# Optimization experiments

Measured on AMD Instinct MI355X. Metric: run time of the kernel, lower is better.

## Reference

```python
import jax, jax.numpy as jnp
import numpy as np

B, S, H, M = 32, 512, 1024, 8  # batch, seq_len, HP_hidden_dim, term_span (max span length)


def setup_inputs() -> dict:
    key = jax.random.key(0)
    ks = jax.random.split(key, 6)
    return {
        "hidden_states": jax.random.normal(ks[0], (B, S, H), jnp.float32),
        "term_weight": jax.random.normal(ks[1], (H,), jnp.float32),          # nn.Parameter termWeight
        "w_in": jax.random.normal(ks[2], (H, H), jnp.float32) / np.float32(np.sqrt(H)),  # TermAttention.linear_in weight
        "b_in": jnp.zeros((H,), jnp.float32),                                 # TermAttention.linear_in bias
        "score_w": jax.random.normal(ks[3], (H,), jnp.float32) / np.float32(np.sqrt(H)),  # spanEmb2Score weight
        "score_b": jnp.zeros((), jnp.float32),                                # spanEmb2Score bias
        "seq_lengths": jnp.full((B,), S, jnp.int32),                          # full-length sentences (K is then static)
        "gold_mask": jax.random.randint(ks[4], (B, S, M), 0, 20, jnp.int32),
    }


def reference(hidden_states, term_weight, w_in, b_in, score_w, score_b, seq_lengths, gold_mask):
    B_, S_, H_ = hidden_states.shape
    M_ = gold_mask.shape[-1]

    # TermAttention: query = linear_in(termWeight)
    query = jnp.dot(w_in, term_weight) + b_in  # [H]

    pos = jnp.arange(S_)[:, None] + jnp.arange(M_)[None, :]          # [S, M]
    win = jnp.take(hidden_states, jnp.clip(pos, 0, S_ - 1), axis=1)  # [B, S, M, H]

    # Attention logits: dot(hidden, query), softmax over span positions per span length l+1
    logits = jnp.einsum('bsmh,h->bsm', win, query)                   # [B, S, M]
    m_idx = jnp.arange(M_)
    pos_mask = m_idx[None, :] < (m_idx[:, None] + 1)                 # [L, M]: position m valid for span length l+1
    masked = jnp.where(pos_mask[None, None], logits[:, :, None, :], -jnp.inf)  # [B, S, L, M]
    att = jax.nn.softmax(masked, axis=-1)
    pooled = jnp.einsum('bslm,bsmh->bslh', att, win)                 # [B, S, L, H] attention-pooled span reps

    # spanEmb2Score: Linear(H, 1)
    scores = jnp.einsum('bslh,h->bsl', pooled, score_w) + score_b    # [B, S, L]

    # Valid (deduplicated) spans: (s, s+l+1) kept iff s + l + 1 <= seq_len (matches set-dedup of clipped ends)
    span_valid = (jnp.arange(S_)[None, :, None] + m_idx[None, None, :] + 1) <= seq_lengths[:, None, None]
    gold = (gold_mask == 0) & span_valid

    # SoftMarginLoss: target 1 for gold spans, target 0 for all other spans -> constant log(2) term (faithful)
    per_span = jnp.where(gold, jax.nn.softplus(-scores), jnp.log(2.0).astype(scores.dtype))
    n_valid = jnp.sum(span_valid).astype(scores.dtype)
    loss = jnp.sum(jnp.where(span_valid, per_span, 0.0)) / n_valid

    # Precision@K, K = floor(0.3 * total_words); static since all sentences are full length
    K = int(0.3 * B_ * S_)
    flat_scores = jnp.where(span_valid, scores, -jnp.inf).reshape(-1)
    _, top_idx = jax.lax.top_k(flat_scores, K)
    right = jnp.sum(gold.reshape(-1)[top_idx])
    precision = right / K
    return loss, precision
```

## Files before the change

### kernel.cpp

```cpp
#include <hip/hip_runtime.h>

#define BB 32
#define SS 512
#define HH 1024
#define MM 8
#define NROWS (BB*SS)
#define NSPANS (BB*SS*MM)
#define KSEL 4915

constexpr size_t OFF_QUERY = 0;
constexpr size_t OFF_QD    = 4096;
constexpr size_t OFF_SD    = OFF_QD + 65536;
constexpr size_t OFF_KEYS  = OFF_SD + 65536;
constexpr size_t OFF_GOLD  = OFF_KEYS + 524288;
constexpr size_t OFF_H0    = OFF_GOLD + 524288;
constexpr size_t OFF_H1    = OFF_H0 + 16384;
constexpr size_t OFF_H2    = OFF_H1 + 16384;
constexpr size_t OFF_SCAL  = OFF_H2 + 1024;
constexpr size_t OFF_EQ    = OFF_SCAL + 64;
constexpr unsigned ZERO_WORDS = (unsigned)((OFF_EQ - OFF_H0) / 4);

struct Scal {
    float    loss_sum;
    unsigned n_valid;
    unsigned right_gt;
    unsigned eq_count;
    unsigned done;
};

__device__ __forceinline__ unsigned sortable_key(float f) {
    unsigned b = __float_as_uint(f);
    return (b & 0x80000000u) ? ~b : (b | 0x80000000u);
}

__device__ __forceinline__ void sel4096(const unsigned* __restrict__ gh, unsigned R,
                                        unsigned* sp, unsigned* sres, int tid,
                                        unsigned& c, unsigned& rem) {
    unsigned loc[16]; unsigned lsumv = 0;
    #pragma unroll
    for (int i = 0; i < 16; ++i) { loc[i] = gh[tid * 16 + i]; lsumv += loc[i]; }
    __syncthreads();
    sp[tid] = lsumv;
    __syncthreads();
    #pragma unroll
    for (int off = 1; off < 256; off <<= 1) {
        unsigned v = (tid + off < 256) ? sp[tid + off] : 0u;
        __syncthreads();
        sp[tid] += v;
        __syncthreads();
    }
    unsigned Pt  = sp[tid];
    unsigned Pt1 = (tid < 255) ? sp[tid + 1] : 0u;
    if (Pt >= R && Pt1 < R) {
        unsigned cum = Pt1;
        #pragma unroll
        for (int i = 15; i >= 0; --i) {
            unsigned h = loc[i];
            if (cum + h >= R) { sres[0] = (unsigned)(tid * 16 + i); sres[1] = R - cum; break; }
            cum += h;
        }
    }
    __syncthreads();
    c = sres[0]; rem = sres[1];
    __syncthreads();
}

__device__ __forceinline__ void sel256(const unsigned* __restrict__ gh, unsigned R,
                                       unsigned* sp, unsigned* sres, int tid,
                                       unsigned& c, unsigned& rem) {
    __syncthreads();
    sp[tid] = gh[tid];
    __syncthreads();
    #pragma unroll
    for (int off = 1; off < 256; off <<= 1) {
        unsigned v = (tid + off < 256) ? sp[tid + off] : 0u;
        __syncthreads();
        sp[tid] += v;
        __syncthreads();
    }
    unsigned Pt  = sp[tid];
    unsigned Pt1 = (tid < 255) ? sp[tid + 1] : 0u;
    if (Pt >= R && Pt1 < R) { sres[0] = (unsigned)tid; sres[1] = R - Pt1; }
    __syncthreads();
    c = sres[0]; rem = sres[1];
    __syncthreads();
}

__global__ void k_query(const float* __restrict__ w_in, const float* __restrict__ tw,
                        const float* __restrict__ b_in, char* __restrict__ ws) {
    if (blockIdx.x == 0) {
        unsigned* z = (unsigned*)(ws + OFF_H0);
        for (unsigned i = threadIdx.x; i < ZERO_WORDS; i += 256) z[i] = 0u;
    }
    float* query = (float*)(ws + OFF_QUERY);
    int wave = (blockIdx.x * blockDim.x + threadIdx.x) >> 6;
    int lane = threadIdx.x & 63;
    if (wave >= HH) return;
    const float4* wrow = (const float4*)(w_in + (size_t)wave * HH);
    const float4* tv   = (const float4*)tw;
    float s = 0.f;
    #pragma unroll
    for (int p = 0; p < 4; ++p) {
        int c = p * 64 + lane;
        float4 w = wrow[c]; float4 t = tv[c];
        s += w.x*t.x + w.y*t.y + w.z*t.z + w.w*t.w;
    }
    #pragma unroll
    for (int o = 32; o > 0; o >>= 1) s += __shfl_down(s, o);
    if (lane == 0) query[wave] = s + b_in[wave];
}

__global__ void k_dots(const float* __restrict__ hs, const float* __restrict__ sw,
                       char* __restrict__ ws) {
    const float* query = (const float*)(ws + OFF_QUERY);
    float* qd = (float*)(ws + OFF_QD);
    float* sd = (float*)(ws + OFF_SD);
    int wave = (blockIdx.x * blockDim.x + threadIdx.x) >> 6;
    int lane = threadIdx.x & 63;
    if (wave >= NROWS) return;
    const float4* row = (const float4*)(hs + (size_t)wave * HH);
    const float4* qv  = (const float4*)query;
    const float4* sv  = (const float4*)sw;
    float a = 0.f, c2 = 0.f;
    #pragma unroll
    for (int p = 0; p < 4; ++p) {
        int c = p * 64 + lane;
        float4 h = row[c]; float4 q = qv[c]; float4 w = sv[c];
        a  += h.x*q.x + h.y*q.y + h.z*q.z + h.w*q.w;
        c2 += h.x*w.x + h.y*w.y + h.z*w.z + h.w*w.w;
    }
    #pragma unroll
    for (int o = 32; o > 0; o >>= 1) { a += __shfl_down(a, o); c2 += __shfl_down(c2, o); }
    if (lane == 0) { qd[wave] = a; sd[wave] = c2; }
}

__global__ void k_scores(const int* __restrict__ gold_mask, const int* __restrict__ seq_lengths,
                         const float* __restrict__ score_b_p, char* __restrict__ ws) {
    const float* qd = (const float*)(ws + OFF_QD);
    const float* sd = (const float*)(ws + OFF_SD);
    unsigned* keys  = (unsigned*)(ws + OFF_KEYS);
    unsigned* goldf = (unsigned*)(ws + OFF_GOLD);
    unsigned* h0    = (unsigned*)(ws + OFF_H0);
    Scal*     sc    = (Scal*)(ws + OFF_SCAL);

    __shared__ unsigned hloc[4096];
    __shared__ float lsum[256];
    __shared__ int   lcnt[256];
    for (int i = threadIdx.x; i < 4096; i += 256) hloc[i] = 0;
    __syncthreads();

    int t = blockIdx.x * 256 + threadIdx.x;
    int b = t >> 9, s = t & (SS - 1);
    int seqlen = seq_lengths[b];
    float sb = *score_b_p;

    uint4 gm0 = ((const uint4*)gold_mask)[t * 2];
    uint4 gm1 = ((const uint4*)gold_mask)[t * 2 + 1];
    unsigned gmv[8] = {gm0.x, gm0.y, gm0.z, gm0.w, gm1.x, gm1.y, gm1.z, gm1.w};

    unsigned kbuf[8], gbuf[8];
    float lloss = 0.f; int lval = 0;
    float maxv = 0.f, den = 0.f, num = 0.f;
    #pragma unroll
    for (int m = 0; m < MM; ++m) {
        int pos = s + m; if (pos > SS - 1) pos = SS - 1;
        float x = qd[b * SS + pos];
        float v = sd[b * SS + pos];
        if (m == 0)         { maxv = x; den = 1.f; num = v; }
        else if (x > maxv)  { float e = expf(maxv - x); den = den * e + 1.f; num = num * e + v; maxv = x; }
        else                { float e = expf(x - maxv); den += e; num += e * v; }
        float score = num / den + sb;
        bool valid = (s + m + 1) <= seqlen;
        bool gold  = valid && (gmv[m] == 0u);
        unsigned key = valid ? sortable_key(score) : 0u;
        kbuf[m] = key;
        gbuf[m] = gold ? 1u : 0u;
        if (valid) {
            atomicAdd(&hloc[key >> 20], 1u);
            lval++;
            float z = -score;
            float sp = (z > 0.f) ? (z + log1pf(expf(-z))) : log1pf(expf(z));
            lloss += gold ? sp : 0.69314718055994531f;
        }
    }
    ((uint4*)keys)[t * 2]      = make_uint4(kbuf[0], kbuf[1], kbuf[2], kbuf[3]);
    ((uint4*)keys)[t * 2 + 1]  = make_uint4(kbuf[4], kbuf[5], kbuf[6], kbuf[7]);
    ((uint4*)goldf)[t * 2]     = make_uint4(gbuf[0], gbuf[1], gbuf[2], gbuf[3]);
    ((uint4*)goldf)[t * 2 + 1] = make_uint4(gbuf[4], gbuf[5], gbuf[6], gbuf[7]);

    lsum[threadIdx.x] = lloss; lcnt[threadIdx.x] = lval;
    __syncthreads();
    for (int i = threadIdx.x; i < 4096; i += 256) {
        unsigned v = hloc[i]; if (v) atomicAdd(&h0[i], v);
    }
    for (int o = 128; o > 0; o >>= 1) {
        if (threadIdx.x < o) { lsum[threadIdx.x] += lsum[threadIdx.x + o]; lcnt[threadIdx.x] += lcnt[threadIdx.x + o]; }
        __syncthreads();
    }
    if (threadIdx.x == 0) {
        atomicAdd(&sc->loss_sum, lsum[0]);
        atomicAdd(&sc->n_valid, (unsigned)lcnt[0]);
    }
}

__global__ void k_lvl1(char* __restrict__ ws) {
    const unsigned* keys = (const unsigned*)(ws + OFF_KEYS);
    const unsigned* h0   = (const unsigned*)(ws + OFF_H0);
    unsigned* h1         = (unsigned*)(ws + OFF_H1);
    __shared__ unsigned hloc[4096];
    __shared__ unsigned sp[256];
    __shared__ unsigned sres[2];
    int tid = threadIdx.x;
    unsigned c0, r0;
    sel4096(h0, KSEL, sp, sres, tid, c0, r0);
    for (int i = tid; i < 4096; i += 256) hloc[i] = 0;
    __syncthreads();
    for (int i = blockIdx.x * 256 + tid; i < NSPANS; i += gridDim.x * 256) {
        unsigned k = keys[i];
        if (k != 0u && (k >> 20) == c0) atomicAdd(&hloc[(k >> 8) & 0xFFFu], 1u);
    }
    __syncthreads();
    for (int i = tid; i < 4096; i += 256) {
        unsigned v = hloc[i]; if (v) atomicAdd(&h1[i], v);
    }
}

__global__ void k_lvl2(char* __restrict__ ws) {
    const unsigned* keys = (const unsigned*)(ws + OFF_KEYS);
    const unsigned* h0   = (const unsigned*)(ws + OFF_H0);
    const unsigned* h1   = (const unsigned*)(ws + OFF_H1);
    unsigned* h2         = (unsigned*)(ws + OFF_H2);
    __shared__ unsigned hloc[256];
    __shared__ unsigned sp[256];
    __shared__ unsigned sres[2];
    int tid = threadIdx.x;
    unsigned c0, r0, c1, r1;
    sel4096(h0, KSEL, sp, sres, tid, c0, r0);
    sel4096(h1, r0,   sp, sres, tid, c1, r1);
    unsigned pref = (c0 << 12) | c1;
    hloc[tid] = 0;
    __syncthreads();
    for (int i = blockIdx.x * 256 + tid; i < NSPANS; i += gridDim.x * 256) {
        unsigned k = keys[i];
        if (k != 0u && (k >> 8) == pref) atomicAdd(&hloc[k & 0xFFu], 1u);
    }
    __syncthreads();
    { unsigned v = hloc[tid]; if (v) atomicAdd(&h2[tid], v); }
}

__global__ void k_count_final(char* __restrict__ ws, float* __restrict__ out) {
    const unsigned* keys  = (const unsigned*)(ws + OFF_KEYS);
    const unsigned* goldf = (const unsigned*)(ws + OFF_GOLD);
    const unsigned* h0    = (const unsigned*)(ws + OFF_H0);
    const unsigned* h1    = (const unsigned*)(ws + OFF_H1);
    const unsigned* h2    = (const unsigned*)(ws + OFF_H2);
    unsigned* eqL         = (unsigned*)(ws + OFF_EQ);
    Scal*     sc          = (Scal*)(ws + OFF_SCAL);
    __shared__ unsigned sp[256];
    __shared__ unsigned sres[2];
    __shared__ unsigned is_last;
    int tid = threadIdx.x;
    unsigned c0, r0, c1, r1, c2, r2;
    sel4096(h0, KSEL, sp, sres, tid, c0, r0);
    sel4096(h1, r0,   sp, sres, tid, c1, r1);
    sel256 (h2, r1,   sp, sres, tid, c2, r2);
    unsigned tau = (c0 << 20) | (c1 << 8) | c2;
    unsigned T   = r2;

    int lgt = 0;
    for (int i = blockIdx.x * 256 + tid; i < NSPANS; i += gridDim.x * 256) {
        unsigned k = keys[i];
        if (k > tau) lgt += (int)goldf[i];
        else if (k == tau) {
            unsigned p = atomicAdd(&sc->eq_count, 1u);
            if (p < 4096) atomicExch(&eqL[p], (unsigned)i);
        }
    }
    #pragma unroll
    for (int o = 32; o > 0; o >>= 1) lgt += __shfl_down(lgt, o);
    if ((tid & 63) == 0 && lgt) atomicAdd(&sc->right_gt, (unsigned)lgt);

    __threadfence();
    __syncthreads();
    if (tid == 0) {
        unsigned prev = atomicAdd(&sc->done, 1u);
        is_last = (prev == gridDim.x - 1) ? 1u : 0u;
    }
    __syncthreads();
    if (is_last && tid == 0) {
        __threadfence();
        unsigned neq = __hip_atomic_load(&sc->eq_count, __ATOMIC_RELAXED, __HIP_MEMORY_SCOPE_AGENT);
        if (neq > 4096) neq = 4096;
        unsigned extra = 0;
        if (T >= neq) {
            for (unsigned i = 0; i < neq; ++i) {
                unsigned v = __hip_atomic_load(&eqL[i], __ATOMIC_RELAXED, __HIP_MEMORY_SCOPE_AGENT);
                extra += goldf[v];
            }
        } else {
            unsigned prev2 = 0; bool first = true;
            for (unsigned it = 0; it < T; ++it) {
                unsigned mn = 0xFFFFFFFFu;
                for (unsigned i = 0; i < neq; ++i) {
                    unsigned v = __hip_atomic_load(&eqL[i], __ATOMIC_RELAXED, __HIP_MEMORY_SCOPE_AGENT);
                    if ((first || v > prev2) && v < mn) mn = v;
                }
                if (mn == 0xFFFFFFFFu) break;
                extra += goldf[mn];
                prev2 = mn; first = false;
            }
        }
        float ls = __hip_atomic_load(&sc->loss_sum, __ATOMIC_RELAXED, __HIP_MEMORY_SCOPE_AGENT);
        unsigned nv = __hip_atomic_load(&sc->n_valid, __ATOMIC_RELAXED, __HIP_MEMORY_SCOPE_AGENT);
        unsigned rg = __hip_atomic_load(&sc->right_gt, __ATOMIC_RELAXED, __HIP_MEMORY_SCOPE_AGENT);
        out[0] = ls / (float)nv;
        out[1] = (float)(rg + extra) / (float)KSEL;
    }
}

extern "C" void kernel_launch(void* const* d_in, const int* in_sizes, int n_in,
                              void* d_out, int out_size, void* d_ws, size_t ws_size,
                              hipStream_t stream) {
    const float* hidden   = (const float*)d_in[0];
    const float* term_w   = (const float*)d_in[1];
    const float* w_in     = (const float*)d_in[2];
    const float* b_in     = (const float*)d_in[3];
    const float* score_w  = (const float*)d_in[4];
    const float* score_b  = (const float*)d_in[5];
    const int*   seq_len  = (const int*)d_in[6];
    const int*   gmask    = (const int*)d_in[7];
    float* out            = (float*)d_out;
    char*  ws             = (char*)d_ws;

    k_query      <<<256, 256, 0, stream>>>(w_in, term_w, b_in, ws);
    k_dots       <<<4096, 256, 0, stream>>>(hidden, score_w, ws);
    k_scores     <<<64, 256, 0, stream>>>(gmask, seq_len, score_b, ws);
    k_lvl1       <<<64, 256, 0, stream>>>(ws);
    k_lvl2       <<<64, 256, 0, stream>>>(ws);
    k_count_final<<<64, 256, 0, stream>>>(ws, out);
}
```

Baseline: 142.7 us.

## Replace three-pass radix select with single compaction pass and one-block final select

```diff
diff --git a/kernel.cpp b/kernel.cpp
--- a/kernel.cpp
+++ b/kernel.cpp
@@ -12,20 +12,17 @@
 constexpr size_t OFF_QD    = 4096;
 constexpr size_t OFF_SD    = OFF_QD + 65536;
 constexpr size_t OFF_KEYS  = OFF_SD + 65536;
-constexpr size_t OFF_GOLD  = OFF_KEYS + 524288;
-constexpr size_t OFF_H0    = OFF_GOLD + 524288;
-constexpr size_t OFF_H1    = OFF_H0 + 16384;
-constexpr size_t OFF_H2    = OFF_H1 + 16384;
-constexpr size_t OFF_SCAL  = OFF_H2 + 1024;
-constexpr size_t OFF_EQ    = OFF_SCAL + 64;
-constexpr unsigned ZERO_WORDS = (unsigned)((OFF_EQ - OFF_H0) / 4);
+constexpr size_t OFF_H0    = OFF_KEYS + 524288;
+constexpr size_t OFF_GH    = OFF_H0 + 16384;
+constexpr size_t OFF_SCAL  = OFF_GH + 16384;
+constexpr size_t OFF_CKEY  = OFF_SCAL + 64;
+constexpr size_t OFF_CIDX  = OFF_CKEY + 524288;
+constexpr unsigned ZERO_WORDS = (unsigned)((OFF_SCAL + 64 - OFF_H0) / 4);
 
 struct Scal {
     float    loss_sum;
     unsigned n_valid;
-    unsigned right_gt;
-    unsigned eq_count;
-    unsigned done;
+    unsigned nB;
 };
 
 __device__ __forceinline__ unsigned sortable_key(float f) {
@@ -139,14 +136,15 @@
     const float* qd = (const float*)(ws + OFF_QD);
     const float* sd = (const float*)(ws + OFF_SD);
     unsigned* keys  = (unsigned*)(ws + OFF_KEYS);
-    unsigned* goldf = (unsigned*)(ws + OFF_GOLD);
     unsigned* h0    = (unsigned*)(ws + OFF_H0);
+    unsigned* gh0   = (unsigned*)(ws + OFF_GH);
     Scal*     sc    = (Scal*)(ws + OFF_SCAL);
 
     __shared__ unsigned hloc[4096];
+    __shared__ unsigned gloc[4096];
     __shared__ float lsum[256];
     __shared__ int   lcnt[256];
-    for (int i = threadIdx.x; i < 4096; i += 256) hloc[i] = 0;
+    for (int i = threadIdx.x; i < 4096; i += 256) { hloc[i] = 0; gloc[i] = 0; }
     __syncthreads();
 
     int t = blockIdx.x * 256 + threadIdx.x;
@@ -158,7 +156,7 @@
     uint4 gm1 = ((const uint4*)gold_mask)[t * 2 + 1];
     unsigned gmv[8] = {gm0.x, gm0.y, gm0.z, gm0.w, gm1.x, gm1.y, gm1.z, gm1.w};
 
-    unsigned kbuf[8], gbuf[8];
+    unsigned kbuf[8];
     float lloss = 0.f; int lval = 0;
     float maxv = 0.f, den = 0.f, num = 0.f;
     #pragma unroll
@@ -174,9 +172,9 @@
         bool gold  = valid && (gmv[m] == 0u);
         unsigned key = valid ? sortable_key(score) : 0u;
         kbuf[m] = key;
-        gbuf[m] = gold ? 1u : 0u;
         if (valid) {
             atomicAdd(&hloc[key >> 20], 1u);
+            if (gold) atomicAdd(&gloc[key >> 20], 1u);
             lval++;
             float z = -score;
             float sp = (z > 0.f) ? (z + log1pf(expf(-z))) : log1pf(expf(z));
@@ -185,13 +183,12 @@
     }
     ((uint4*)keys)[t * 2]      = make_uint4(kbuf[0], kbuf[1], kbuf[2], kbuf[3]);
     ((uint4*)keys)[t * 2 + 1]  = make_uint4(kbuf[4], kbuf[5], kbuf[6], kbuf[7]);
-    ((uint4*)goldf)[t * 2]     = make_uint4(gbuf[0], gbuf[1], gbuf[2], gbuf[3]);
-    ((uint4*)goldf)[t * 2 + 1] = make_uint4(gbuf[4], gbuf[5], gbuf[6], gbuf[7]);
 
     lsum[threadIdx.x] = lloss; lcnt[threadIdx.x] = lval;
     __syncthreads();
     for (int i = threadIdx.x; i < 4096; i += 256) {
         unsigned v = hloc[i]; if (v) atomicAdd(&h0[i], v);
+        unsigned g = gloc[i]; if (g) atomicAdd(&gh0[i], g);
     }
     for (int o = 128; o > 0; o >>= 1) {
         if (threadIdx.x < o) { lsum[threadIdx.x] += lsum[threadIdx.x + o]; lcnt[threadIdx.x] += lcnt[threadIdx.x + o]; }
@@ -203,118 +200,126 @@
     }
 }
 
-__global__ void k_lvl1(char* __restrict__ ws) {
+__global__ void k_compact(char* __restrict__ ws, const int* __restrict__ gold_mask) {
     const unsigned* keys = (const unsigned*)(ws + OFF_KEYS);
     const unsigned* h0   = (const unsigned*)(ws + OFF_H0);
-    unsigned* h1         = (unsigned*)(ws + OFF_H1);
-    __shared__ unsigned hloc[4096];
+    unsigned* ckey       = (unsigned*)(ws + OFF_CKEY);
+    unsigned* cidx       = (unsigned*)(ws + OFF_CIDX);
+    Scal*     sc         = (Scal*)(ws + OFF_SCAL);
     __shared__ unsigned sp[256];
     __shared__ unsigned sres[2];
     int tid = threadIdx.x;
     unsigned c0, r0;
     sel4096(h0, KSEL, sp, sres, tid, c0, r0);
-    for (int i = tid; i < 4096; i += 256) hloc[i] = 0;
-    __syncthreads();
-    for (int i = blockIdx.x * 256 + tid; i < NSPANS; i += gridDim.x * 256) {
+    int lane = tid & 63;
+    for (int i = blockIdx.x * 256 + tid; i < NSPANS; i += 64 * 256) {
         unsigned k = keys[i];
-        if (k != 0u && (k >> 20) == c0) atomicAdd(&hloc[(k >> 8) & 0xFFFu], 1u);
-    }
-    __syncthreads();
-    for (int i = tid; i < 4096; i += 256) {
-        unsigned v = hloc[i]; if (v) atomicAdd(&h1[i], v);
-    }
-}
-
-__global__ void k_lvl2(char* __restrict__ ws) {
-    const unsigned* keys = (const unsigned*)(ws + OFF_KEYS);
+        bool match = (k >> 20) == c0;
+        unsigned long long m = __ballot(match);
+        if (m) {
+            int leader = __ffsll(m) - 1;
+            unsigned base = 0;
+            if (lane == leader) base = atomicAdd(&sc->nB, (unsigned)__popcll(m));
+            base = __shfl(base, leader);
+            if (match) {
+                unsigned pos = base + (unsigned)__popcll(m & ((1ull << lane) - 1ull));
+                ckey[pos] = k & 0xFFFFFu;
+                unsigned gold = (gold_mask[i] == 0) ? 1u : 0u;
+                cidx[pos] = ((unsigned)i << 1) | gold;
+            }
+        }
+    }
+}
+
+__global__ void k_final(char* __restrict__ ws, float* __restrict__ out) {
     const unsigned* h0   = (const unsigned*)(ws + OFF_H0);
-    const unsigned* h1   = (const unsigned*)(ws + OFF_H1);
-    unsigned* h2         = (unsigned*)(ws + OFF_H2);
-    __shared__ unsigned hloc[256];
+    const unsigned* gh0  = (const unsigned*)(ws + OFF_GH);
+    const unsigned* ckey = (const unsigned*)(ws + OFF_CKEY);
+    const unsigned* cidx = (const unsigned*)(ws + OFF_CIDX);
+    Scal*     sc         = (Scal*)(ws + OFF_SCAL);
+
+    __shared__ unsigned hloc[4096];
+    __shared__ unsigned tie[4096];
     __shared__ unsigned sp[256];
     __shared__ unsigned sres[2];
+    __shared__ unsigned red[256];
+    __shared__ unsigned tcnt;
     int tid = threadIdx.x;
-    unsigned c0, r0, c1, r1;
+
+    unsigned c0, r0;
     sel4096(h0, KSEL, sp, sres, tid, c0, r0);
-    sel4096(h1, r0,   sp, sres, tid, c1, r1);
-    unsigned pref = (c0 << 12) | c1;
+
+    unsigned g = 0;
+    #pragma unroll
+    for (int i = 0; i < 16; ++i) {
+        unsigned bin = (unsigned)(tid * 16 + i);
+        if (bin > c0) g += gh0[bin];
+    }
+    red[tid] = g;
+    __syncthreads();
+    for (int o = 128; o > 0; o >>= 1) {
+        if (tid < o) red[tid] += red[tid + o];
+        __syncthreads();
+    }
+    unsigned gAbove = red[0];
+    unsigned nB = sc->nB;
+
+    for (int i = tid; i < 4096; i += 256) hloc[i] = 0;
+    __syncthreads();
+    for (unsigned j = tid; j < nB; j += 256) atomicAdd(&hloc[ckey[j] >> 8], 1u);
+    __syncthreads();
+    unsigned c1, r1;
+    sel4096(hloc, r0, sp, sres, tid, c1, r1);
+
     hloc[tid] = 0;
     __syncthreads();
-    for (int i = blockIdx.x * 256 + tid; i < NSPANS; i += gridDim.x * 256) {
-        unsigned k = keys[i];
-        if (k != 0u && (k >> 8) == pref) atomicAdd(&hloc[k & 0xFFu], 1u);
-    }
-    __syncthreads();
-    { unsigned v = hloc[tid]; if (v) atomicAdd(&h2[tid], v); }
-}
-
-__global__ void k_count_final(char* __restrict__ ws, float* __restrict__ out) {
-    const unsigned* keys  = (const unsigned*)(ws + OFF_KEYS);
-    const unsigned* goldf = (const unsigned*)(ws + OFF_GOLD);
-    const unsigned* h0    = (const unsigned*)(ws + OFF_H0);
-    const unsigned* h1    = (const unsigned*)(ws + OFF_H1);
-    const unsigned* h2    = (const unsigned*)(ws + OFF_H2);
-    unsigned* eqL         = (unsigned*)(ws + OFF_EQ);
-    Scal*     sc          = (Scal*)(ws + OFF_SCAL);
-    __shared__ unsigned sp[256];
-    __shared__ unsigned sres[2];
-    __shared__ unsigned is_last;
-    int tid = threadIdx.x;
-    unsigned c0, r0, c1, r1, c2, r2;
-    sel4096(h0, KSEL, sp, sres, tid, c0, r0);
-    sel4096(h1, r0,   sp, sres, tid, c1, r1);
-    sel256 (h2, r1,   sp, sres, tid, c2, r2);
-    unsigned tau = (c0 << 20) | (c1 << 8) | c2;
-    unsigned T   = r2;
-
-    int lgt = 0;
-    for (int i = blockIdx.x * 256 + tid; i < NSPANS; i += gridDim.x * 256) {
-        unsigned k = keys[i];
-        if (k > tau) lgt += (int)goldf[i];
-        else if (k == tau) {
-            unsigned p = atomicAdd(&sc->eq_count, 1u);
-            if (p < 4096) atomicExch(&eqL[p], (unsigned)i);
-        }
-    }
-    #pragma unroll
-    for (int o = 32; o > 0; o >>= 1) lgt += __shfl_down(lgt, o);
-    if ((tid & 63) == 0 && lgt) atomicAdd(&sc->right_gt, (unsigned)lgt);
-
-    __threadfence();
-    __syncthreads();
+    for (unsigned j = tid; j < nB; j += 256) {
+        unsigned ck = ckey[j];
+        if ((ck >> 8) == c1) atomicAdd(&hloc[ck & 0xFFu], 1u);
+    }
+    __syncthreads();
+    unsigned c2, T;
+    sel256(hloc, r1, sp, sres, tid, c2, T);
+    unsigned tauL = (c1 << 8) | c2;
+
+    if (tid == 0) tcnt = 0;
+    __syncthreads();
+    unsigned gb = 0;
+    for (unsigned j = tid; j < nB; j += 256) {
+        unsigned ck = ckey[j];
+        if (ck > tauL) gb += cidx[j] & 1u;
+        else if (ck == tauL) {
+            unsigned p = atomicAdd(&tcnt, 1u);
+            if (p < 4096) tie[p] = cidx[j];
+        }
+    }
+    red[tid] = gb;
+    __syncthreads();
+    for (int o = 128; o > 0; o >>= 1) {
+        if (tid < o) red[tid] += red[tid + o];
+        __syncthreads();
+    }
     if (tid == 0) {
-        unsigned prev = atomicAdd(&sc->done, 1u);
-        is_last = (prev == gridDim.x - 1) ? 1u : 0u;
-    }
-    __syncthreads();
-    if (is_last && tid == 0) {
-        __threadfence();
-        unsigned neq = __hip_atomic_load(&sc->eq_count, __ATOMIC_RELAXED, __HIP_MEMORY_SCOPE_AGENT);
-        if (neq > 4096) neq = 4096;
+        unsigned gBnd = red[0];
+        unsigned neq = tcnt; if (neq > 4096) neq = 4096;
         unsigned extra = 0;
         if (T >= neq) {
-            for (unsigned i = 0; i < neq; ++i) {
-                unsigned v = __hip_atomic_load(&eqL[i], __ATOMIC_RELAXED, __HIP_MEMORY_SCOPE_AGENT);
-                extra += goldf[v];
-            }
+            for (unsigned i = 0; i < neq; ++i) extra += tie[i] & 1u;
         } else {
-            unsigned prev2 = 0; bool first = true;
+            unsigned prev = 0; bool first = true;
             for (unsigned it = 0; it < T; ++it) {
-                unsigned mn = 0xFFFFFFFFu;
+                unsigned mn = 0xFFFFFFFFu; unsigned mng = 0;
                 for (unsigned i = 0; i < neq; ++i) {
-                    unsigned v = __hip_atomic_load(&eqL[i], __ATOMIC_RELAXED, __HIP_MEMORY_SCOPE_AGENT);
-                    if ((first || v > prev2) && v < mn) mn = v;
+                    unsigned v = tie[i]; unsigned idx = v >> 1;
+                    if ((first || idx > prev) && idx < mn) { mn = idx; mng = v & 1u; }
                 }
                 if (mn == 0xFFFFFFFFu) break;
-                extra += goldf[mn];
-                prev2 = mn; first = false;
+                extra += mng;
+                prev = mn; first = false;
             }
         }
-        float ls = __hip_atomic_load(&sc->loss_sum, __ATOMIC_RELAXED, __HIP_MEMORY_SCOPE_AGENT);
-        unsigned nv = __hip_atomic_load(&sc->n_valid, __ATOMIC_RELAXED, __HIP_MEMORY_SCOPE_AGENT);
-        unsigned rg = __hip_atomic_load(&sc->right_gt, __ATOMIC_RELAXED, __HIP_MEMORY_SCOPE_AGENT);
-        out[0] = ls / (float)nv;
-        out[1] = (float)(rg + extra) / (float)KSEL;
+        out[0] = sc->loss_sum / (float)sc->n_valid;
+        out[1] = (float)(gAbove + gBnd + extra) / (float)KSEL;
     }
 }
 
@@ -332,10 +337,9 @@
     float* out            = (float*)d_out;
     char*  ws             = (char*)d_ws;
 
-    k_query      <<<256, 256, 0, stream>>>(w_in, term_w, b_in, ws);
-    k_dots       <<<4096, 256, 0, stream>>>(hidden, score_w, ws);
-    k_scores     <<<64, 256, 0, stream>>>(gmask, seq_len, score_b, ws);
-    k_lvl1       <<<64, 256, 0, stream>>>(ws);
-    k_lvl2       <<<64, 256, 0, stream>>>(ws);
-    k_count_final<<<64, 256, 0, stream>>>(ws, out);
-}
+    k_query  <<<256, 256, 0, stream>>>(w_in, term_w, b_in, ws);
+    k_dots   <<<4096, 256, 0, stream>>>(hidden, score_w, ws);
+    k_scores <<<64, 256, 0, stream>>>(gmask, seq_len, score_b, ws);
+    k_compact<<<64, 256, 0, stream>>>(ws, gmask);
+    k_final  <<<1, 256, 0, stream>>>(ws, out);
+}
```

Result: faster. 136.4 us (-4.4%).
